# Kernel tuning notes

Hardware: AMD Instinct MI355X
Metric: run time of the kernel (lower is better)

The kernel has to match this reference:

```python
import jax, jax.numpy as jnp
import numpy as np

N = 50000
LN_EPS = 1e-5
NEG_SLOPE = 0.2


def layer_norm(x, w, b):
    mu = jnp.mean(x, axis=-1, keepdims=True)
    var = jnp.mean((x - mu) ** 2, axis=-1, keepdims=True)
    return (x - mu) * jax.lax.rsqrt(var + LN_EPS) * w + b


def gat_conv(x, src, dst, W, a_src, a_dst, bias, concat):
    # W: [in, H*D]; a_src/a_dst: [H, D]
    H, D = a_src.shape
    h = (x @ W).reshape(-1, H, D)                      # [N, H, D]
    s = jnp.einsum('nhd,hd->nh', h, a_src)             # alpha contribution of source
    t = jnp.einsum('nhd,hd->nh', h, a_dst)             # alpha contribution of target
    e = jax.nn.leaky_relu(s[src] + t[dst], NEG_SLOPE)  # [E, H] edge logits
    m = jax.ops.segment_max(e, dst, num_segments=N)    # segment softmax over incoming edges
    p = jnp.exp(e - m[dst])
    z = jax.ops.segment_sum(p, dst, num_segments=N)
    alpha = p / (z[dst] + 1e-16)                       # [E, H]
    out = jax.ops.segment_sum(alpha[:, :, None] * h[src], dst, num_segments=N)  # [N, H, D]
    out = out.reshape(N, H * D) if concat else out.mean(axis=1)
    return out + bias


def setup_inputs() -> dict:
    key = jax.random.key(0)
    ks = jax.random.split(key, 16)
    IN, HID, OUT, H1, H2 = 256, 32, 40, 6, 3
    E = 800000
    g = lambda k, shp, fan: jax.random.normal(k, shp, jnp.float32) * (1.0 / np.sqrt(fan))
    inp = {
        'x': jax.random.normal(ks[0], (N, IN), jnp.float32),
        'edge_index': jax.random.randint(ks[1], (2, E), 0, N, jnp.int32),
        'W1': g(ks[2], (IN, H1 * HID), IN), 'a1s': g(ks[3], (H1, HID), HID), 'a1d': g(ks[4], (H1, HID), HID),
        'b1': jnp.zeros((H1 * HID,), jnp.float32),
        'ln1w': jnp.ones((H1 * HID,), jnp.float32), 'ln1b': jnp.zeros((H1 * HID,), jnp.float32),
        'W2': g(ks[5], (H1 * HID, H2 * HID), H1 * HID), 'a2s': g(ks[6], (H2, HID), HID), 'a2d': g(ks[7], (H2, HID), HID),
        'b2': jnp.zeros((H2 * HID,), jnp.float32),
        'ln2w': jnp.ones((H2 * HID,), jnp.float32), 'ln2b': jnp.zeros((H2 * HID,), jnp.float32),
        'W3': g(ks[8], (H2 * HID, 1 * OUT), H2 * HID), 'a3s': g(ks[9], (1, OUT), OUT), 'a3d': g(ks[10], (1, OUT), OUT),
        'b3': jnp.zeros((OUT,), jnp.float32),
        'ln3w': jnp.ones((OUT,), jnp.float32), 'ln3b': jnp.zeros((OUT,), jnp.float32),
    }
    return inp


def reference(x, edge_index, W1, a1s, a1d, b1, ln1w, ln1b,
              W2, a2s, a2d, b2, ln2w, ln2b,
              W3, a3s, a3d, b3, ln3w, ln3b):
    # add self-loops (PyG GATConv default); eval mode -> dropouts are identity
    loop = jnp.arange(N, dtype=edge_index.dtype)
    src = jnp.concatenate([edge_index[0], loop])
    dst = jnp.concatenate([edge_index[1], loop])

    h = gat_conv(x, src, dst, W1, a1s, a1d, b1, concat=True)
    h = jax.nn.elu(layer_norm(h, ln1w, ln1b))
    h = gat_conv(h, src, dst, W2, a2s, a2d, b2, concat=True)
    h = jax.nn.elu(layer_norm(h, ln2w, ln2b))
    h = gat_conv(h, src, dst, W3, a3s, a3d, b3, concat=False)
    h = layer_norm(h, ln3w, ln3b)
    return jax.nn.log_softmax(h, axis=1)
```

## Files before the change

kernel.cpp:

```cpp
#include <hip/hip_runtime.h>
#include <hip/hip_bf16.h>
#include <cstdint>

#define NNODES 50000
#define NEDGES 800000
#define ETOT   (NEDGES + NNODES)
#define LN_EPS 1e-5f
#define NEG_SLOPE 0.2f
#define ELLW   64

typedef __attribute__((ext_vector_type(8))) short s16x8;
typedef __attribute__((ext_vector_type(4))) float f32x4;

__device__ __forceinline__ float bf2f(unsigned short u) {
    return __uint_as_float(((unsigned int)u) << 16);
}
__device__ __forceinline__ unsigned short f2bf(float f) {
    unsigned int u = __float_as_uint(f);
    u += 0x7FFFu + ((u >> 16) & 1u);
    return (unsigned short)(u >> 16);
}
__device__ __forceinline__ float plo32(unsigned u) { return __uint_as_float(u << 16); }
__device__ __forceinline__ float phi32(unsigned u) { return __uint_as_float(u & 0xffff0000u); }


#define W1SZ (192 * 256)
#define W2SZ (96 * 192)
#define W3SZ (48 * 96)

__global__ __launch_bounds__(256) void prep_kernel(const float* __restrict__ W1, const float* __restrict__ W2,
                                                   const float* __restrict__ W3, unsigned short* __restrict__ wt1,
                                                   unsigned short* __restrict__ wt2, unsigned short* __restrict__ wt3,
                                                   int* __restrict__ counts, int* __restrict__ ell) {
    int i = blockIdx.x * 256 + threadIdx.x;
    if (i < NNODES) {
        counts[i] = 1;
        ell[i * ELLW] = i;
    }
    if (i < W1SZ) {
        int c = i >> 8, k = i & 255;
        int n = c >> 4, r = c & 15;
        wt1[((n * 32 + (k >> 3)) * 16 + r) * 8 + (k & 7)] = f2bf(W1[k * 192 + c]);
    } else if (i < W1SZ + W2SZ) {
        int j = i - W1SZ;
        int c = j / 192, k = j - c * 192;
        int n = c >> 4, r = c & 15;
        wt2[((n * 24 + (k >> 3)) * 16 + r) * 8 + (k & 7)] = f2bf(W2[k * 96 + c]);
    } else if (i < W1SZ + W2SZ + W3SZ) {
        int j = i - (W1SZ + W2SZ);
        int c = j / 96, k = j - c * 96;
        int n = c >> 4, r = c & 15;
        wt3[((n * 12 + (k >> 3)) * 16 + r) * 8 + (k & 7)] = (c < 40) ? f2bf(W3[k * 40 + c]) : (unsigned short)0;
    }
}


template<int K, int F, int CS, int FP, int H, int D, int SPAD, bool ABF, bool FILL>
__global__ __launch_bounds__(256) void gemmst_kernel(const void* __restrict__ Xv,
                                                     const unsigned short* __restrict__ Wt,
                                                     unsigned short* __restrict__ C,
                                                     const float* __restrict__ asf, const float* __restrict__ adf,
                                                     float* __restrict__ sbuf, float* __restrict__ tbuf,
                                                     int nrows, int gblocks,
                                                     const int* __restrict__ eidx, int* counts,
                                                     int* __restrict__ ell, int e) {
    if constexpr (FILL) {
        if (blockIdx.x >= (unsigned)gblocks) {
            int i = ((int)blockIdx.x - gblocks) * 256 + (int)threadIdx.x;
            if (i < e) {
                int sv = eidx[i];
                int d  = eidx[e + i];
                int slot = atomicAdd(&counts[d], 1);
                if (slot < ELLW) ell[d * ELLW + slot] = sv;
            }
            return;
        }
    }
    constexpr int NT = FP / 16;
    int gw = (blockIdx.x * 256 + threadIdx.x) >> 6;
    int lane = threadIdx.x & 63;
    int mbase = gw * 16;
    if (mbase >= nrows) return;
    const int r = lane & 15;
    const int q = lane >> 4;

    f32x4 acc[NT];
#pragma unroll
    for (int n = 0; n < NT; ++n) acc[n] = (f32x4){0.f, 0.f, 0.f, 0.f};

    int arow = mbase + r;
    if (arow >= nrows) arow = nrows - 1;
    const unsigned short* xb = (const unsigned short*)Xv + (size_t)arow * K;
    const float* xf = (const float*)Xv + (size_t)arow * K;

    for (int k0 = 0; k0 < K; k0 += 32) {
        const int kk = k0 + q * 8;
        const unsigned kc = (unsigned)(kk >> 3);
        s16x8 a;
        if constexpr (ABF) {
            a = *reinterpret_cast<const s16x8*>(xb + kk);
        } else {
            float4 lo = *reinterpret_cast<const float4*>(xf + kk);
            float4 hi = *reinterpret_cast<const float4*>(xf + kk + 4);
            a[0] = (short)f2bf(lo.x); a[1] = (short)f2bf(lo.y);
            a[2] = (short)f2bf(lo.z); a[3] = (short)f2bf(lo.w);
            a[4] = (short)f2bf(hi.x); a[5] = (short)f2bf(hi.y);
            a[6] = (short)f2bf(hi.z); a[7] = (short)f2bf(hi.w);
        }
#pragma unroll
        for (int n = 0; n < NT; ++n) {
            s16x8 b = *reinterpret_cast<const s16x8*>(Wt + (((unsigned)n * (K / 8) + kc) * 16 + (unsigned)r) * 8);
            acc[n] = __builtin_amdgcn_mfma_f32_16x16x32_bf16(a, b, acc[n], 0, 0, 0);
        }
    }

#pragma unroll
    for (int n = 0; n < NT; ++n) {
        int col = n * 16 + r;
        if (col < F) {
#pragma unroll
            for (int i = 0; i < 4; ++i) {
                int row = mbase + q * 4 + i;
                if (row < nrows) C[(size_t)row * CS + col] = f2bf(acc[n][i]);
            }
        }
    }

    float ps[4][H], pt[4][H];
#pragma unroll
    for (int i = 0; i < 4; ++i)
#pragma unroll
        for (int hh = 0; hh < H; ++hh) { ps[i][hh] = 0.f; pt[i][hh] = 0.f; }
#pragma unroll
    for (int n = 0; n < NT; ++n) {
        constexpr int NCOL = 1;
        (void)NCOL;
        const int col = n * 16 + r;
        const int h = (n * 16) / D;
        float av = (col < F) ? asf[col] : 0.f;
        float dv = (col < F) ? adf[col] : 0.f;
#pragma unroll
        for (int i = 0; i < 4; ++i) {
            ps[i][h] = fmaf(acc[n][i], av, ps[i][h]);
            pt[i][h] = fmaf(acc[n][i], dv, pt[i][h]);
        }
    }
#pragma unroll
    for (int off = 1; off <= 8; off <<= 1) {
#pragma unroll
        for (int i = 0; i < 4; ++i)
#pragma unroll
            for (int hh = 0; hh < H; ++hh) {
                ps[i][hh] += __shfl_xor(ps[i][hh], off);
                pt[i][hh] += __shfl_xor(pt[i][hh], off);
            }
    }
#pragma unroll
    for (int hh = 0; hh < H; ++hh) {
        if (r == hh) {
#pragma unroll
            for (int i = 0; i < 4; ++i) {
                int row = mbase + q * 4 + i;
                if (row < nrows) {
                    sbuf[row * SPAD + hh] = ps[i][hh];
                    tbuf[row * H + hh]    = pt[i][hh];
                }
            }
        }
    }
}


template<int H, int D, int FS, int CPL, int SPAD, int MODE, typename OutT>
__global__ __launch_bounds__(256) void agg7_kernel(const unsigned short* __restrict__ feat,
                                                   const float* __restrict__ sb, const float* __restrict__ tb,
                                                   const int* __restrict__ counts, const int* __restrict__ ell,
                                                   const float* __restrict__ bias, const float* __restrict__ lnw,
                                                   const float* __restrict__ lnb, OutT* __restrict__ out, int n) {
    constexpr int F = H * D;
    constexpr int NL = F / CPL;
    int wid = (blockIdx.x * blockDim.x + threadIdx.x) >> 6;
    int lane = threadIdx.x & 63;
    if (wid >= n) return;
    const int node = wid;
    const int base = node * ELLW;
    int cnt = counts[node];
    if (cnt > ELLW) cnt = ELLW;
    const bool act = lane < NL;
    const unsigned ch0 = (unsigned)(lane < NL ? lane : 0) * CPL;
    const int h = (int)(ch0 / D);
    const float th = tb[node * H + h];

    float z = 0.f;
    float acc[CPL];
#pragma unroll
    for (int c = 0; c < CPL; ++c) acc[c] = 0.f;

    auto pval = [&](float sv) -> float {
        float e = sv + th;
        e = fmaxf(e, NEG_SLOPE * e);
        return __expf(e);
    };
    auto fmae = [&](float p, const unsigned short* fp) {
        if constexpr (CPL == 4) {
            uint2 w = *reinterpret_cast<const uint2*>(fp);
            acc[0] = fmaf(p, plo32(w.x), acc[0]);
            acc[1] = fmaf(p, phi32(w.x), acc[1]);
            acc[2] = fmaf(p, plo32(w.y), acc[2]);
            acc[3] = fmaf(p, phi32(w.y), acc[3]);
        } else if constexpr (CPL == 2) {
            unsigned w = *reinterpret_cast<const unsigned*>(fp);
            acc[0] = fmaf(p, plo32(w), acc[0]);
            acc[1] = fmaf(p, phi32(w), acc[1]);
        } else {
            acc[0] = fmaf(p, bf2f(*fp), acc[0]);
        }
    };

    int j = 0;
    for (; j + 7 < cnt; j += 8) {
        int4 snA = *reinterpret_cast<const int4*>(ell + base + j);
        int4 snB = *reinterpret_cast<const int4*>(ell + base + j + 4);
        unsigned o0 = (unsigned)snA.x * FS + ch0;
        unsigned o1 = (unsigned)snA.y * FS + ch0;
        unsigned o2 = (unsigned)snA.z * FS + ch0;
        unsigned o3 = (unsigned)snA.w * FS + ch0;
        unsigned o4 = (unsigned)snB.x * FS + ch0;
        unsigned o5 = (unsigned)snB.y * FS + ch0;
        unsigned o6 = (unsigned)snB.z * FS + ch0;
        unsigned o7 = (unsigned)snB.w * FS + ch0;
        if (act) {
            float s0 = sb[(unsigned)snA.x * SPAD + h];
            float s1 = sb[(unsigned)snA.y * SPAD + h];
            float s2 = sb[(unsigned)snA.z * SPAD + h];
            float s3 = sb[(unsigned)snA.w * SPAD + h];
            float s4 = sb[(unsigned)snB.x * SPAD + h];
            float s5 = sb[(unsigned)snB.y * SPAD + h];
            float s6 = sb[(unsigned)snB.z * SPAD + h];
            float s7 = sb[(unsigned)snB.w * SPAD + h];
            if constexpr (CPL == 4) {
                uint2 w0 = *reinterpret_cast<const uint2*>(feat + o0);
                uint2 w1 = *reinterpret_cast<const uint2*>(feat + o1);
                uint2 w2 = *reinterpret_cast<const uint2*>(feat + o2);
                uint2 w3 = *reinterpret_cast<const uint2*>(feat + o3);
                uint2 w4 = *reinterpret_cast<const uint2*>(feat + o4);
                uint2 w5 = *reinterpret_cast<const uint2*>(feat + o5);
                uint2 w6 = *reinterpret_cast<const uint2*>(feat + o6);
                uint2 w7 = *reinterpret_cast<const uint2*>(feat + o7);
                float p0 = pval(s0), p1 = pval(s1), p2 = pval(s2), p3 = pval(s3);
                float p4 = pval(s4), p5 = pval(s5), p6 = pval(s6), p7 = pval(s7);
                z += ((p0 + p1) + (p2 + p3)) + ((p4 + p5) + (p6 + p7));
                acc[0] = fmaf(p0, plo32(w0.x), acc[0]); acc[1] = fmaf(p0, phi32(w0.x), acc[1]);
                acc[2] = fmaf(p0, plo32(w0.y), acc[2]); acc[3] = fmaf(p0, phi32(w0.y), acc[3]);
                acc[0] = fmaf(p1, plo32(w1.x), acc[0]); acc[1] = fmaf(p1, phi32(w1.x), acc[1]);
                acc[2] = fmaf(p1, plo32(w1.y), acc[2]); acc[3] = fmaf(p1, phi32(w1.y), acc[3]);
                acc[0] = fmaf(p2, plo32(w2.x), acc[0]); acc[1] = fmaf(p2, phi32(w2.x), acc[1]);
                acc[2] = fmaf(p2, plo32(w2.y), acc[2]); acc[3] = fmaf(p2, phi32(w2.y), acc[3]);
                acc[0] = fmaf(p3, plo32(w3.x), acc[0]); acc[1] = fmaf(p3, phi32(w3.x), acc[1]);
                acc[2] = fmaf(p3, plo32(w3.y), acc[2]); acc[3] = fmaf(p3, phi32(w3.y), acc[3]);
                acc[0] = fmaf(p4, plo32(w4.x), acc[0]); acc[1] = fmaf(p4, phi32(w4.x), acc[1]);
                acc[2] = fmaf(p4, plo32(w4.y), acc[2]); acc[3] = fmaf(p4, phi32(w4.y), acc[3]);
                acc[0] = fmaf(p5, plo32(w5.x), acc[0]); acc[1] = fmaf(p5, phi32(w5.x), acc[1]);
                acc[2] = fmaf(p5, plo32(w5.y), acc[2]); acc[3] = fmaf(p5, phi32(w5.y), acc[3]);
                acc[0] = fmaf(p6, plo32(w6.x), acc[0]); acc[1] = fmaf(p6, phi32(w6.x), acc[1]);
                acc[2] = fmaf(p6, plo32(w6.y), acc[2]); acc[3] = fmaf(p6, phi32(w6.y), acc[3]);
                acc[0] = fmaf(p7, plo32(w7.x), acc[0]); acc[1] = fmaf(p7, phi32(w7.x), acc[1]);
                acc[2] = fmaf(p7, plo32(w7.y), acc[2]); acc[3] = fmaf(p7, phi32(w7.y), acc[3]);
            } else if constexpr (CPL == 2) {
                unsigned w0 = *reinterpret_cast<const unsigned*>(feat + o0);
                unsigned w1 = *reinterpret_cast<const unsigned*>(feat + o1);
                unsigned w2 = *reinterpret_cast<const unsigned*>(feat + o2);
                unsigned w3 = *reinterpret_cast<const unsigned*>(feat + o3);
                unsigned w4 = *reinterpret_cast<const unsigned*>(feat + o4);
                unsigned w5 = *reinterpret_cast<const unsigned*>(feat + o5);
                unsigned w6 = *reinterpret_cast<const unsigned*>(feat + o6);
                unsigned w7 = *reinterpret_cast<const unsigned*>(feat + o7);
                float p0 = pval(s0), p1 = pval(s1), p2 = pval(s2), p3 = pval(s3);
                float p4 = pval(s4), p5 = pval(s5), p6 = pval(s6), p7 = pval(s7);
                z += ((p0 + p1) + (p2 + p3)) + ((p4 + p5) + (p6 + p7));
                acc[0] = fmaf(p0, plo32(w0), acc[0]); acc[1] = fmaf(p0, phi32(w0), acc[1]);
                acc[0] = fmaf(p1, plo32(w1), acc[0]); acc[1] = fmaf(p1, phi32(w1), acc[1]);
                acc[0] = fmaf(p2, plo32(w2), acc[0]); acc[1] = fmaf(p2, phi32(w2), acc[1]);
                acc[0] = fmaf(p3, plo32(w3), acc[0]); acc[1] = fmaf(p3, phi32(w3), acc[1]);
                acc[0] = fmaf(p4, plo32(w4), acc[0]); acc[1] = fmaf(p4, phi32(w4), acc[1]);
                acc[0] = fmaf(p5, plo32(w5), acc[0]); acc[1] = fmaf(p5, phi32(w5), acc[1]);
                acc[0] = fmaf(p6, plo32(w6), acc[0]); acc[1] = fmaf(p6, phi32(w6), acc[1]);
                acc[0] = fmaf(p7, plo32(w7), acc[0]); acc[1] = fmaf(p7, phi32(w7), acc[1]);
            } else {
                unsigned short w0 = feat[o0], w1 = feat[o1], w2 = feat[o2], w3 = feat[o3];
                unsigned short w4 = feat[o4], w5 = feat[o5], w6 = feat[o6], w7 = feat[o7];
                float p0 = pval(s0), p1 = pval(s1), p2 = pval(s2), p3 = pval(s3);
                float p4 = pval(s4), p5 = pval(s5), p6 = pval(s6), p7 = pval(s7);
                z += ((p0 + p1) + (p2 + p3)) + ((p4 + p5) + (p6 + p7));
                acc[0] = fmaf(p0, bf2f(w0), acc[0]);
                acc[0] = fmaf(p1, bf2f(w1), acc[0]);
                acc[0] = fmaf(p2, bf2f(w2), acc[0]);
                acc[0] = fmaf(p3, bf2f(w3), acc[0]);
                acc[0] = fmaf(p4, bf2f(w4), acc[0]);
                acc[0] = fmaf(p5, bf2f(w5), acc[0]);
                acc[0] = fmaf(p6, bf2f(w6), acc[0]);
                acc[0] = fmaf(p7, bf2f(w7), acc[0]);
            }
        }
    }
    for (; j + 3 < cnt; j += 4) {
        int4 snA = *reinterpret_cast<const int4*>(ell + base + j);
        if (act) {
            float p0 = pval(sb[(unsigned)snA.x * SPAD + h]);
            float p1 = pval(sb[(unsigned)snA.y * SPAD + h]);
            float p2 = pval(sb[(unsigned)snA.z * SPAD + h]);
            float p3 = pval(sb[(unsigned)snA.w * SPAD + h]);
            z += (p0 + p1) + (p2 + p3);
            fmae(p0, feat + (unsigned)snA.x * FS + ch0);
            fmae(p1, feat + (unsigned)snA.y * FS + ch0);
            fmae(p2, feat + (unsigned)snA.z * FS + ch0);
            fmae(p3, feat + (unsigned)snA.w * FS + ch0);
        }
    }
    for (; j < cnt; ++j) {
        int sn = ell[base + j];
        if (act) {
            float p = pval(sb[(unsigned)sn * SPAD + h]);
            z += p;
            fmae(p, feat + (unsigned)sn * FS + ch0);
        }
    }

    const float zinv = 1.f / (z + 1e-16f);
    float v[CPL];
    float sum = 0.f, sumsq = 0.f;
#pragma unroll
    for (int c = 0; c < CPL; ++c) v[c] = 0.f;
    if (act) {
#pragma unroll
        for (int c = 0; c < CPL; ++c) {
            v[c] = fmaf(acc[c], zinv, bias[ch0 + c]);
            sum += v[c];
            sumsq += v[c] * v[c];
        }
    }
#pragma unroll
    for (int off = 32; off; off >>= 1) {
        sum += __shfl_xor(sum, off);
        sumsq += __shfl_xor(sumsq, off);
    }
    const float mu = sum / F;
    const float var = sumsq / F - mu * mu;
    const float rstd = rsqrtf(var + LN_EPS);

    if (MODE == 0) {
        if (act) {
            unsigned short yb[CPL];
#pragma unroll
            for (int c = 0; c < CPL; ++c) {
                float y = (v[c] - mu) * rstd * lnw[ch0 + c] + lnb[ch0 + c];
                y = y > 0.f ? y : expm1f(y);
                yb[c] = f2bf(y);
            }
            OutT* op = out + (size_t)node * F + ch0;
            if constexpr (CPL == 4) {
                ushort4 st = {yb[0], yb[1], yb[2], yb[3]};
                *reinterpret_cast<ushort4*>(op) = st;
            } else if constexpr (CPL == 2) {
                ushort2 st = {yb[0], yb[1]};
                *reinterpret_cast<ushort2*>(op) = st;
            } else {
                *op = yb[0];
            }
        }
    } else {
        float y = 0.f, mx = -1e30f;
        if (act) {
            y = (v[0] - mu) * rstd * lnw[ch0] + lnb[ch0];
            mx = y;
        }
#pragma unroll
        for (int off = 32; off; off >>= 1) mx = fmaxf(mx, __shfl_xor(mx, off));
        float se = act ? __expf(y - mx) : 0.f;
#pragma unroll
        for (int off = 32; off; off >>= 1) se += __shfl_xor(se, off);
        float lse = logf(se);
        if (act) ((float*)out)[(size_t)node * F + ch0] = y - mx - lse;
    }
}


static inline size_t align_up(size_t x) { return (x + 255) & ~(size_t)255; }

extern "C" void kernel_launch(void* const* d_in, const int* in_sizes, int n_in,
                              void* d_out, int out_size, void* d_ws, size_t ws_size,
                              hipStream_t stream) {
    const float* x    = (const float*)d_in[0];
    const int*   eidx = (const int*)d_in[1];
    const float* W1   = (const float*)d_in[2];
    const float* a1s  = (const float*)d_in[3];
    const float* a1d  = (const float*)d_in[4];
    const float* b1   = (const float*)d_in[5];
    const float* ln1w = (const float*)d_in[6];
    const float* ln1b = (const float*)d_in[7];
    const float* W2   = (const float*)d_in[8];
    const float* a2s  = (const float*)d_in[9];
    const float* a2d  = (const float*)d_in[10];
    const float* b2   = (const float*)d_in[11];
    const float* ln2w = (const float*)d_in[12];
    const float* ln2b = (const float*)d_in[13];
    const float* W3   = (const float*)d_in[14];
    const float* a3s  = (const float*)d_in[15];
    const float* a3d  = (const float*)d_in[16];
    const float* b3   = (const float*)d_in[17];
    const float* ln3w = (const float*)d_in[18];
    const float* ln3b = (const float*)d_in[19];

    char* w = (char*)d_ws;
    int* counts = (int*)w;  w += align_up((size_t)NNODES * 4);
    int* ell    = (int*)w;  w += align_up((size_t)NNODES * ELLW * 4);
    unsigned short* bufA = (unsigned short*)w; w += align_up((size_t)NNODES * 192 * 2);
    unsigned short* bufB = (unsigned short*)w; w += align_up((size_t)NNODES * 192 * 2);
    float* sbuf = (float*)w; w += align_up((size_t)NNODES * 8 * 4);
    float* tbuf = (float*)w; w += align_up((size_t)NNODES * 8 * 4);
    unsigned short* wt1 = (unsigned short*)w; w += align_up((size_t)W1SZ * 2);
    unsigned short* wt2 = (unsigned short*)w; w += align_up((size_t)W2SZ * 2);
    unsigned short* wt3 = (unsigned short*)w; w += align_up((size_t)W3SZ * 2);

    const int BS = 256;
    const int PREP_N = W1SZ + W2SZ + W3SZ;
    prep_kernel<<<(PREP_N + BS - 1) / BS, BS, 0, stream>>>(W1, W2, W3, wt1, wt2, wt3, counts, ell);

    const int GRID_MM  = ((NNODES + 15) / 16 + 3) / 4;
    const int FILL_NB  = (NEDGES + BS - 1) / BS;
    const int GRID_AGG = (NNODES + 3) / 4;

    gemmst_kernel<256, 192, 192, 192, 6, 32, 8, false, true>
        <<<GRID_MM + FILL_NB, BS, 0, stream>>>(x, wt1, bufA, a1s, a1d, sbuf, tbuf, NNODES,
                                               GRID_MM, eidx, counts, ell, NEDGES);
    agg7_kernel<6, 32, 192, 4, 8, 0, unsigned short><<<GRID_AGG, BS, 0, stream>>>(bufA, sbuf, tbuf, counts, ell, b1, ln1w, ln1b, bufB, NNODES);

    gemmst_kernel<192, 96, 128, 96, 3, 32, 4, true, false>
        <<<GRID_MM, BS, 0, stream>>>(bufB, wt2, bufA, a2s, a2d, sbuf, tbuf, NNODES,
                                     GRID_MM, nullptr, nullptr, nullptr, 0);
    agg7_kernel<3, 32, 128, 2, 4, 0, unsigned short><<<GRID_AGG, BS, 0, stream>>>(bufA, sbuf, tbuf, counts, ell, b2, ln2w, ln2b, bufB, NNODES);

    gemmst_kernel<96, 40, 64, 48, 1, 40, 1, true, false>
        <<<GRID_MM, BS, 0, stream>>>(bufB, wt3, bufA, a3s, a3d, sbuf, tbuf, NNODES,
                                     GRID_MM, nullptr, nullptr, nullptr, 0);
    agg7_kernel<1, 40, 64, 1, 1, 1, float><<<GRID_AGG, BS, 0, stream>>>(bufA, sbuf, tbuf, counts, ell, b3, ln3w, ln3b, (float*)d_out, NNODES);
}
```

Baseline: 274.9 us.

## Split GEMM column tiles across warps and reduce attention scores in LDS

Adds a WSPLIT template parameter so several waves share one 16-row tile, each computing a subset of the output column tiles. This cuts accumulator registers per wave and raises the number of waves working on the first two projection GEMMs. Per-head source/target score partials are combined with LDS atomics and block barriers before being written out. Launch bounds now request higher occupancy and the K loop is unrolled by two. The cost is extra LDS traffic, synchronisation, and A-row reloads by every wave that shares a tile.

```diff
diff --git a/kernel.cpp b/kernel.cpp
--- a/kernel.cpp
+++ b/kernel.cpp
@@ -55,15 +55,15 @@
 }
 
 
-template<int K, int F, int CS, int FP, int H, int D, int SPAD, bool ABF, bool FILL>
-__global__ __launch_bounds__(256) void gemmst_kernel(const void* __restrict__ Xv,
-                                                     const unsigned short* __restrict__ Wt,
-                                                     unsigned short* __restrict__ C,
-                                                     const float* __restrict__ asf, const float* __restrict__ adf,
-                                                     float* __restrict__ sbuf, float* __restrict__ tbuf,
-                                                     int nrows, int gblocks,
-                                                     const int* __restrict__ eidx, int* counts,
-                                                     int* __restrict__ ell, int e) {
+template<int K, int F, int CS, int FP, int H, int D, int SPAD, int WSPLIT, bool ABF, bool FILL>
+__global__ __launch_bounds__(256, 6) void gemmst_kernel(const void* __restrict__ Xv,
+                                                        const unsigned short* __restrict__ Wt,
+                                                        unsigned short* __restrict__ C,
+                                                        const float* __restrict__ asf, const float* __restrict__ adf,
+                                                        float* __restrict__ sbuf, float* __restrict__ tbuf,
+                                                        int nrows, int gblocks,
+                                                        const int* __restrict__ eidx, int* counts,
+                                                        int* __restrict__ ell, int e) {
     if constexpr (FILL) {
         if (blockIdx.x >= (unsigned)gblocks) {
             int i = ((int)blockIdx.x - gblocks) * 256 + (int)threadIdx.x;
@@ -76,23 +76,37 @@
             return;
         }
     }
-    constexpr int NT = FP / 16;
-    int gw = (blockIdx.x * 256 + threadIdx.x) >> 6;
-    int lane = threadIdx.x & 63;
-    int mbase = gw * 16;
-    if (mbase >= nrows) return;
+    constexpr int NT  = FP / 16;
+    constexpr int NTW = NT / WSPLIT;
+    constexpr int TPB = 4 / WSPLIT;
+
+    __shared__ float lds_s[TPB][16][H];
+    __shared__ float lds_t[TPB][16][H];
+
+    const int w    = threadIdx.x >> 6;
+    const int lane = threadIdx.x & 63;
+    const int tile = w / WSPLIT;
+    const int sub  = w % WSPLIT;
+    const int pb   = sub * NTW;
+    const int mbase = ((int)blockIdx.x * TPB + tile) * 16;
     const int r = lane & 15;
     const int q = lane >> 4;
 
-    f32x4 acc[NT];
-#pragma unroll
-    for (int n = 0; n < NT; ++n) acc[n] = (f32x4){0.f, 0.f, 0.f, 0.f};
+    if constexpr (WSPLIT == 1) {
+        if (mbase >= nrows) return;
+    }
+
+    f32x4 acc[NTW];
+#pragma unroll
+    for (int nn = 0; nn < NTW; ++nn) acc[nn] = (f32x4){0.f, 0.f, 0.f, 0.f};
 
     int arow = mbase + r;
     if (arow >= nrows) arow = nrows - 1;
+    if (arow < 0) arow = 0;
     const unsigned short* xb = (const unsigned short*)Xv + (size_t)arow * K;
     const float* xf = (const float*)Xv + (size_t)arow * K;
 
+#pragma unroll 2
     for (int k0 = 0; k0 < K; k0 += 32) {
         const int kk = k0 + q * 8;
         const unsigned kc = (unsigned)(kk >> 3);
@@ -108,20 +122,21 @@
             a[6] = (short)f2bf(hi.z); a[7] = (short)f2bf(hi.w);
         }
 #pragma unroll
-        for (int n = 0; n < NT; ++n) {
-            s16x8 b = *reinterpret_cast<const s16x8*>(Wt + (((unsigned)n * (K / 8) + kc) * 16 + (unsigned)r) * 8);
-            acc[n] = __builtin_amdgcn_mfma_f32_16x16x32_bf16(a, b, acc[n], 0, 0, 0);
-        }
-    }
-
-#pragma unroll
-    for (int n = 0; n < NT; ++n) {
-        int col = n * 16 + r;
+        for (int nn = 0; nn < NTW; ++nn) {
+            const unsigned gn = (unsigned)(pb + nn);
+            s16x8 b = *reinterpret_cast<const s16x8*>(Wt + ((gn * (K / 8) + kc) * 16 + (unsigned)r) * 8);
+            acc[nn] = __builtin_amdgcn_mfma_f32_16x16x32_bf16(a, b, acc[nn], 0, 0, 0);
+        }
+    }
+
+#pragma unroll
+    for (int nn = 0; nn < NTW; ++nn) {
+        int col = (pb + nn) * 16 + r;
         if (col < F) {
 #pragma unroll
             for (int i = 0; i < 4; ++i) {
                 int row = mbase + q * 4 + i;
-                if (row < nrows) C[(size_t)row * CS + col] = f2bf(acc[n][i]);
+                if (row < nrows) C[(size_t)row * CS + col] = f2bf(acc[nn][i]);
             }
         }
     }
@@ -132,17 +147,20 @@
 #pragma unroll
         for (int hh = 0; hh < H; ++hh) { ps[i][hh] = 0.f; pt[i][hh] = 0.f; }
 #pragma unroll
-    for (int n = 0; n < NT; ++n) {
-        constexpr int NCOL = 1;
-        (void)NCOL;
-        const int col = n * 16 + r;
-        const int h = (n * 16) / D;
-        float av = (col < F) ? asf[col] : 0.f;
-        float dv = (col < F) ? adf[col] : 0.f;
-#pragma unroll
-        for (int i = 0; i < 4; ++i) {
-            ps[i][h] = fmaf(acc[n][i], av, ps[i][h]);
-            pt[i][h] = fmaf(acc[n][i], dv, pt[i][h]);
+    for (int ss = 0; ss < WSPLIT; ++ss) {
+        if (ss != sub) continue;
+#pragma unroll
+        for (int nn = 0; nn < NTW; ++nn) {
+            const int gn = ss * NTW + nn;
+            const int col = gn * 16 + r;
+            const int h = (gn * 16) / D;
+            float av = (col < F) ? asf[col] : 0.f;
+            float dv = (col < F) ? adf[col] : 0.f;
+#pragma unroll
+            for (int i = 0; i < 4; ++i) {
+                ps[i][h] = fmaf(acc[nn][i], av, ps[i][h]);
+                pt[i][h] = fmaf(acc[nn][i], dv, pt[i][h]);
+            }
         }
     }
 #pragma unroll
@@ -155,16 +173,49 @@
                 pt[i][hh] += __shfl_xor(pt[i][hh], off);
             }
     }
-#pragma unroll
-    for (int hh = 0; hh < H; ++hh) {
-        if (r == hh) {
-#pragma unroll
-            for (int i = 0; i < 4; ++i) {
-                int row = mbase + q * 4 + i;
-                if (row < nrows) {
-                    sbuf[row * SPAD + hh] = ps[i][hh];
-                    tbuf[row * H + hh]    = pt[i][hh];
+
+    if constexpr (WSPLIT == 1) {
+#pragma unroll
+        for (int hh = 0; hh < H; ++hh) {
+            if (r == hh) {
+#pragma unroll
+                for (int i = 0; i < 4; ++i) {
+                    int row = mbase + q * 4 + i;
+                    if (row < nrows) {
+                        sbuf[row * SPAD + hh] = ps[i][hh];
+                        tbuf[row * H + hh]    = pt[i][hh];
+                    }
                 }
+            }
+        }
+    } else {
+        constexpr int NE = TPB * 16 * H;
+        if ((int)threadIdx.x < NE) {
+            int idx = threadIdx.x;
+            int t2 = idx / (16 * H), rem = idx % (16 * H);
+            lds_s[t2][rem / H][rem % H] = 0.f;
+            lds_t[t2][rem / H][rem % H] = 0.f;
+        }
+        __syncthreads();
+#pragma unroll
+        for (int hh = 0; hh < H; ++hh) {
+            if (r == hh) {
+#pragma unroll
+                for (int i = 0; i < 4; ++i) {
+                    atomicAdd(&lds_s[tile][q * 4 + i][hh], ps[i][hh]);
+                    atomicAdd(&lds_t[tile][q * 4 + i][hh], pt[i][hh]);
+                }
+            }
+        }
+        __syncthreads();
+        if ((int)threadIdx.x < NE) {
+            int idx = threadIdx.x;
+            int t2 = idx / (16 * H), rem = idx % (16 * H);
+            int rw = rem / H, hh = rem % H;
+            int row = (int)blockIdx.x * TPB * 16 + t2 * 16 + rw;
+            if (row < nrows) {
+                sbuf[row * SPAD + hh] = lds_s[t2][rw][hh];
+                tbuf[row * H + hh]    = lds_t[t2][rw][hh];
             }
         }
     }
@@ -426,22 +477,24 @@
     const int PREP_N = W1SZ + W2SZ + W3SZ;
     prep_kernel<<<(PREP_N + BS - 1) / BS, BS, 0, stream>>>(W1, W2, W3, wt1, wt2, wt3, counts, ell);
 
-    const int GRID_MM  = ((NNODES + 15) / 16 + 3) / 4;
+    const int G1 = NNODES / 16;
+    const int G2 = (NNODES + 31) / 32;
+    const int G3 = (NNODES + 63) / 64;
     const int FILL_NB  = (NEDGES + BS - 1) / BS;
     const int GRID_AGG = (NNODES + 3) / 4;
 
-    gemmst_kernel<256, 192, 192, 192, 6, 32, 8, false, true>
-        <<<GRID_MM + FILL_NB, BS, 0, stream>>>(x, wt1, bufA, a1s, a1d, sbuf, tbuf, NNODES,
-                                               GRID_MM, eidx, counts, ell, NEDGES);
+    gemmst_kernel<256, 192, 192, 192, 6, 32, 8, 4, false, true>
+        <<<G1 + FILL_NB, BS, 0, stream>>>(x, wt1, bufA, a1s, a1d, sbuf, tbuf, NNODES,
+                                          G1, eidx, counts, ell, NEDGES);
     agg7_kernel<6, 32, 192, 4, 8, 0, unsigned short><<<GRID_AGG, BS, 0, stream>>>(bufA, sbuf, tbuf, counts, ell, b1, ln1w, ln1b, bufB, NNODES);
 
-    gemmst_kernel<192, 96, 128, 96, 3, 32, 4, true, false>
-        <<<GRID_MM, BS, 0, stream>>>(bufB, wt2, bufA, a2s, a2d, sbuf, tbuf, NNODES,
-                                     GRID_MM, nullptr, nullptr, nullptr, 0);
+    gemmst_kernel<192, 96, 128, 96, 3, 32, 4, 2, true, false>
+        <<<G2, BS, 0, stream>>>(bufB, wt2, bufA, a2s, a2d, sbuf, tbuf, NNODES,
+                                G2, nullptr, nullptr, nullptr, 0);
     agg7_kernel<3, 32, 128, 2, 4, 0, unsigned short><<<GRID_AGG, BS, 0, stream>>>(bufA, sbuf, tbuf, counts, ell, b2, ln2w, ln2b, bufB, NNODES);
 
-    gemmst_kernel<96, 40, 64, 48, 1, 40, 1, true, false>
-        <<<GRID_MM, BS, 0, stream>>>(bufB, wt3, bufA, a3s, a3d, sbuf, tbuf, NNODES,
-                                     GRID_MM, nullptr, nullptr, nullptr, 0);
+    gemmst_kernel<96, 40, 64, 48, 1, 40, 1, 1, true, false>
+        <<<G3, BS, 0, stream>>>(bufB, wt3, bufA, a3s, a3d, sbuf, tbuf, NNODES,
+                                G3, nullptr, nullptr, nullptr, 0);
     agg7_kernel<1, 40, 64, 1, 1, 1, float><<<GRID_AGG, BS, 0, stream>>>(bufA, sbuf, tbuf, counts, ell, b3, ln3w, ln3b, (float*)d_out, NNODES);
 }
```

Result: slower. 280.8 us (+2.1%).
